# Kernel tuning notes

Measured on AMD Instinct MI355X. Metric: run time of the kernel, lower is better.

## Reference

```python
import jax, jax.numpy as jnp
import numpy as np

EPS = 1e-6
R_DEPTH = 12   # CONFIG['max_recursion_depth']
STACK = 48     # CONFIG['stack_size']
GB, CG, CC = 0.8, 2.0, 0.25  # graph_bias_scale, context_gate_strength, commitment_cost


def _g(k, shape, s=0.05):
    return (jax.random.normal(k, shape) * s).astype(jnp.float32)


def setup_inputs():
    D, V, B, S = 128, 16384, 32, 128
    NS, NM = 64, 128
    ks = iter(jax.random.split(jax.random.key(0), 40))
    return {
        "input_ids": jax.random.randint(next(ks), (B, S), 0, V),
        "prev_syn_idx": jax.random.randint(next(ks), (B,), 0, NS),
        "prev_sem_idx": jax.random.randint(next(ks), (B,), 0, NM),
        "emb_mag": _g(next(ks), (V, D), 1.0),
        "emb_phase": _g(next(ks), (V, D), 1.0),
        "cell_Wr": _g(next(ks), (D, D)), "cell_Wi": _g(next(ks), (D, D)),
        "norm_scale": jnp.ones((D,), jnp.float32),
        "norm_shift": jnp.zeros((D,), jnp.float32),
        "modrelu_b": jnp.zeros((D,), jnp.float32),
        "qWr": _g(next(ks), (D, D)), "qWi": _g(next(ks), (D, D)),
        "kWr": _g(next(ks), (D, D)), "kWi": _g(next(ks), (D, D)),
        "vWr": _g(next(ks), (D, D)), "vWi": _g(next(ks), (D, D)),
        "oWr": _g(next(ks), (D, D)), "oWi": _g(next(ks), (D, D)),
        "halt_W": _g(next(ks), (2 * D, 1)),
        "halt_b": jnp.full((1,), -2.0, jnp.float32),  # nn.init.constant_(halt_linear.bias, -2.0)
        "stk_W": _g(next(ks), (2 * D, 3)), "stk_b": jnp.zeros((3,), jnp.float32),
        "cb_syn": _g(next(ks), (64, 2 * D), 1.0),
        "cb_sem": _g(next(ks), (128, 2 * D), 1.0),
        "ctxsyn_W": _g(next(ks), (2 * D, NS)), "ctxsyn_b": jnp.zeros((NS,), jnp.float32),
        "ctxsem_W": _g(next(ks), (2 * D, NM)), "ctxsem_b": jnp.zeros((NM,), jnp.float32),
        "adj_syn": _g(next(ks), (NS, NS), 1.0),
        "adj_sem": _g(next(ks), (NM, NM), 1.0),
        "gate_W": _g(next(ks), (4 * D, D)), "gate_b": jnp.zeros((D,), jnp.float32),
        "dec_W": _g(next(ks), (2 * D, V)), "dec_b": jnp.zeros((V,), jnp.float32),
    }


def _forward(fl, input_ids, prev_syn_idx, prev_sem_idx):
    (emb_mag, emb_phase, cell_Wr, cell_Wi, norm_scale, norm_shift, modrelu_b,
     qWr, qWi, kWr, kWi, vWr, vWi, oWr, oWi, halt_W, halt_b, stk_W, stk_b,
     cb_syn, cb_sem, ctxsyn_W, ctxsyn_b, ctxsem_W, ctxsem_b, adj_syn, adj_sem,
     gate_W, gate_b, dec_W, dec_b) = fl
    B = input_ids.shape[0]
    D = emb_mag.shape[1]
    sg = jax.lax.stop_gradient

    def clin(r, i, Wr, Wi):  # ComplexLinear (no bias)
        return r @ Wr - i @ Wi, i @ Wr + r @ Wi

    def cell(zr, zi):  # AdaptiveRecursiveCell
        r, i = clin(zr, zi, cell_Wr, cell_Wi)
        # ComplexLayerNorm (torch.var is unbiased -> ddof=1)
        mag = jnp.sqrt(r * r + i * i) + EPS
        mean = mag.mean(-1, keepdims=True)
        var = jnp.var(mag, axis=-1, ddof=1, keepdims=True)
        nm = (mag - mean) / jnp.sqrt(var + EPS) * norm_scale + norm_shift
        r, i = nm * r / mag, nm * i / mag  # cos/sin of original phase
        # ModReLU
        n = jnp.sqrt(r * r + i * i) + EPS
        s = jax.nn.relu(n + modrelu_b) / n
        r, i = r * s, i * s
        # MultiHeadComplexAttention: source computes Q,K but out = V -> o_proj(v_proj(z))
        vr, vi = clin(r, i, vWr, vWi)
        r, i = clin(vr, vi, oWr, oWi)
        zf = jnp.concatenate([r, i], -1)
        halt = jax.nn.sigmoid(zf @ halt_W + halt_b)          # [B,1]
        ctrl = jax.nn.softmax(zf @ stk_W + stk_b, axis=-1)   # [B,3]
        return r, i, halt, ctrl

    def stack_step(zr, zi, mem, ptr, ctrl):  # DifferentiableStack
        push, pop, noop = ctrl[:, 0:1], ctrl[:, 1:2], ctrl[:, 2:3]
        pu, pd = jnp.roll(ptr, 1, axis=1), jnp.roll(ptr, -1, axis=1)
        nptr = push * pu + pop * pd + noop * ptr
        nptr = nptr / (nptr.sum(1, keepdims=True) + EPS)
        zf = jnp.concatenate([zr, zi], -1)
        wm = (push * pu)[:, :, None]                          # write mask [B,STACK,1]
        mem = wm * zf[:, None, :] + mem * (1.0 - wm)
        read = (mem * nptr[:, :, None]).sum(1)                # [B,2D]
        return read[:, :D], read[:, D:], mem, nptr

    def gres(zr, zi, sr, si):  # GatedResidual, g_c = g + i*g
        g = jax.nn.sigmoid(jnp.concatenate([zr, zi, sr, si], -1) @ gate_W + gate_b)
        return ((1.0 - g) * zr + g * zi + g * (sr - si),
                (1.0 - g) * zi - g * zr + g * (si + sr))

    def vq(zr, zi, cb, adj, cW, cbias, pidx):  # ContextAwareDualVQ.vq_step (eval mode)
        zf = jnp.concatenate([zr, zi], -1)                    # [B,2D]
        d = (zf * zf).sum(1, keepdims=True) + (cb * cb).sum(1) - 2.0 * zf @ cb.T
        d = d - GB * jax.nn.sigmoid(adj[pidx]) - CG * jax.nn.softmax(zf @ cW + cbias, -1)
        idx = jnp.argmin(d, axis=1)
        zq = cb[idx]
        loss = jnp.mean((sg(zq) - zf) ** 2) + CC * jnp.mean((zq - sg(zf)) ** 2)
        return zf + sg(zq - zf), loss, idx                    # STE

    def step(carry, ids_t):
        mem, ptr, psyn, psem, lacc = carry
        r, th = emb_mag[ids_t], emb_phase[ids_t]              # embed
        zr, zi = r * jnp.cos(th), r * jnp.sin(th)
        rem = jnp.ones((B, 1), zr.dtype)
        accr = jnp.zeros_like(zr); acci = jnp.zeros_like(zi)
        slr = jnp.zeros_like(zr); sli = jnp.zeros_like(zi)
        for n in range(R_DEPTH):  # ACT recursion, halting-weighted accumulation
            pr, pi, halt, ctrl = cell(zr, zi)
            rr, ri, mem, ptr = stack_step(pr, pi, mem, ptr, ctrl)
            zr, zi = gres(pr, pi, rr, ri)
            w = rem if n == R_DEPTH - 1 else rem * halt
            accr, acci = accr + w * zr, acci + w * zi
            rem = rem * (1.0 - halt)
            slr, sli = slr + zr / R_DEPTH, sli + zi / R_DEPTH
        zqs, ls, isyn = vq(accr, acci, cb_syn, adj_syn, ctxsyn_W, ctxsyn_b, psyn)
        zqm, lm, isem = vq(slr, sli, cb_sem, adj_sem, ctxsem_W, ctxsem_b, psem)
        logits = 0.5 * (zqs + zqm) @ dec_W + dec_b            # decoder: Linear(2D, V)
        return (mem, ptr, isyn, isem, lacc + ls + lm), logits

    mem0 = jnp.zeros((B, STACK, 2 * D), jnp.float32)
    ptr0 = jnp.zeros((B, STACK), jnp.float32).at[:, 0].set(1.0)
    carry0 = (mem0, ptr0, prev_syn_idx, prev_sem_idx, jnp.zeros((), jnp.float32))
    (_, _, _, _, vq_loss), logits = jax.lax.scan(step, carry0, input_ids.T)
    return jnp.transpose(logits, (1, 0, 2)), vq_loss          # [B,S,V], scalar


def reference(input_ids, prev_syn_idx, prev_sem_idx, emb_mag, emb_phase, cell_Wr, cell_Wi, norm_scale, norm_shift, modrelu_b, qWr, qWi, kWr, kWi, vWr, vWi, oWr, oWi, halt_W, halt_b, stk_W, stk_b, cb_syn, cb_sem, ctxsyn_W, ctxsyn_b, ctxsem_W, ctxsem_b, adj_syn, adj_sem, gate_W, gate_b, dec_W, dec_b):
    fl = (emb_mag, emb_phase, cell_Wr, cell_Wi, norm_scale, norm_shift, modrelu_b,
          qWr, qWi, kWr, kWi, vWr, vWi, oWr, oWi, halt_W, halt_b, stk_W, stk_b,
          cb_syn, cb_sem, ctxsyn_W, ctxsyn_b, ctxsem_W, ctxsem_b, adj_syn, adj_sem,
          gate_W, gate_b, dec_W, dec_b)
    return _forward(fl, input_ids, prev_syn_idx, prev_sem_idx)
```

## Files before the change

### kernel.cpp

```cpp
#include <hip/hip_runtime.h>
#include <hip/hip_fp16.h>
#include <math.h>

#define D 128
#define D2 256
#define STK 48
#define SEQ 128
#define BATCH 32
#define RDPT 12
#define NSYN 64
#define NSEM 128
#define VOC 16384
#define EPSF 1e-6f
#define GB_C 0.8f
#define CG_C 2.0f

struct RParams {
  const int* input_ids;
  const int* prev_syn;
  const int* prev_sem;
  const float* emb_mag;
  const float* emb_phase;
  const float* cell_Wr;
  const float* cell_Wi;
  const float* norm_scale;
  const float* norm_shift;
  const float* modrelu_b;
  const float* VOr;
  const float* VOi;
  const float* halt_W;
  const float* halt_b;
  const float* stk_W;
  const float* stk_b;
  const float* cb_syn;
  const float* cb_sem;
  const float* ctxsyn_W;
  const float* ctxsyn_b;
  const float* ctxsem_W;
  const float* ctxsem_b;
  const float* gate_b;
  const uint4* gatePk;
  const float* cbT_syn;
  const float* cbT_sem;
  const float* cnrm_syn;
  const float* cnrm_sem;
  const float* gbsig_syn;
  const float* gbsig_sem;
  float* X;
  float* lossp;
};

__device__ __forceinline__ float waveAllSum(float v) {
  #pragma unroll
  for (int m = 32; m; m >>= 1) v += __shfl_xor(v, m);
  return v;
}

__global__ __launch_bounds__(512, 2) void recur_kernel(RParams p) {
  __shared__ uint4 gateLds[64 * D];
  __shared__ float partr[512], parti[512];
  __shared__ alignas(16) float xr_[D], xi_[D], cr_[D], ci_[D];
  __shared__ float rAiA[D2], marr[D];
  __shared__ alignas(16) float zfc[D2], rd_[D2];
  __shared__ alignas(16) float acc2[D2], sl2[D2];
  __shared__ float zqs[D2];
  __shared__ float sptr[STK];
  __shared__ alignas(16) float nptrs[STK], wms[STK];
  __shared__ float hW_s[D2];
  __shared__ float stW_s[D2 * 3];
  __shared__ float scal[16];
  __shared__ int icb[2];
  __shared__ int ids[SEQ];

  const int tid = threadIdx.x;
  const int b = blockIdx.x;
  const int wv = tid >> 6;
  const int l = tid & 63;
  const int j = tid & 127;
  const int kq = tid >> 7;
  const int k0 = kq * 32;

  float cwr[32], cwi[32], owr[32], owi[32];
  #pragma unroll
  for (int kk = 0; kk < 32; ++kk) {
    cwr[kk] = p.cell_Wr[(size_t)(k0 + kk) * D + j];
    cwi[kk] = p.cell_Wi[(size_t)(k0 + kk) * D + j];
    owr[kk] = p.VOr[(size_t)(k0 + kk) * D + j];
    owi[kk] = p.VOi[(size_t)(k0 + kk) * D + j];
  }
  for (int e = tid; e < 64 * D; e += 512) gateLds[e] = p.gatePk[e];
  float snsR = 0.f, nshR = 0.f, smbR = 0.f, sgbR = 0.f;
  if (tid < D) {
    snsR = p.norm_scale[tid];
    nshR = p.norm_shift[tid];
    smbR = p.modrelu_b[tid];
    sgbR = p.gate_b[tid];
  }
  if (tid < D2) hW_s[tid] = p.halt_W[tid];
  for (int e = tid; e < D2 * 3; e += 512) stW_s[e] = p.stk_W[e];
  if (tid < SEQ) ids[tid] = p.input_ids[(size_t)b * SEQ + tid];
  if (tid < STK) sptr[tid] = (tid == 0) ? 1.f : 0.f;
  if (tid == 0) { icb[0] = p.prev_syn[b]; icb[1] = p.prev_sem[b]; }
  const float hb = p.halt_b[0];
  const float sb0 = p.stk_b[0], sb1 = p.stk_b[1], sb2 = p.stk_b[2];

  float memv[24];
  #pragma unroll
  for (int q = 0; q < 24; ++q) memv[q] = 0.f;
  const int mdl = tid & 255, mjh = tid >> 8;
  float lossAcc = 0.f;
  float remv = 1.f;
  float mNxt = 0.f, pNxt = 0.f;
  __syncthreads();

  if (tid < D) {
    const int id0 = ids[0];
    mNxt = p.emb_mag[(size_t)id0 * D + tid];
    pNxt = p.emb_phase[(size_t)id0 * D + tid];
  }

  for (int t = 0; t < SEQ; ++t) {
    if (tid < D) {
      float sv, cv;
      sincosf(pNxt, &sv, &cv);
      xr_[tid] = mNxt * cv;
      xi_[tid] = mNxt * sv;
    }
    float accR = 0.f, accI = 0.f, slR = 0.f, slI = 0.f;
    if (tid < 64) remv = 1.f;
    __syncthreads();

    for (int n = 0; n < RDPT; ++n) {
      {
        const float4* x4r = (const float4*)(&xr_[k0]);
        const float4* x4i = (const float4*)(&xi_[k0]);
        float a0 = 0.f, a1 = 0.f, a2 = 0.f, a3 = 0.f;
        #pragma unroll
        for (int q = 0; q < 8; ++q) {
          float4 xa = x4r[q];
          float4 xb = x4i[q];
          a0 = fmaf(xa.x, cwr[q*4+0], a0); a0 = fmaf(-xb.x, cwi[q*4+0], a0);
          a1 = fmaf(xb.x, cwr[q*4+0], a1); a1 = fmaf(xa.x, cwi[q*4+0], a1);
          a2 = fmaf(xa.y, cwr[q*4+1], a2); a2 = fmaf(-xb.y, cwi[q*4+1], a2);
          a3 = fmaf(xb.y, cwr[q*4+1], a3); a3 = fmaf(xa.y, cwi[q*4+1], a3);
          a0 = fmaf(xa.z, cwr[q*4+2], a0); a0 = fmaf(-xb.z, cwi[q*4+2], a0);
          a1 = fmaf(xb.z, cwr[q*4+2], a1); a1 = fmaf(xa.z, cwi[q*4+2], a1);
          a2 = fmaf(xa.w, cwr[q*4+3], a2); a2 = fmaf(-xb.w, cwi[q*4+3], a2);
          a3 = fmaf(xb.w, cwr[q*4+3], a3); a3 = fmaf(xa.w, cwi[q*4+3], a3);
        }
        partr[tid] = a0 + a2;
        parti[tid] = a1 + a3;
      }
      __syncthreads();
      if (tid < D) {
        float rr = partr[tid] + partr[tid + 128] + partr[tid + 256] + partr[tid + 384];
        float ii = parti[tid] + parti[tid + 128] + parti[tid + 256] + parti[tid + 384];
        rAiA[tid] = rr;
        rAiA[tid + 128] = ii;
        marr[tid] = sqrtf(rr * rr + ii * ii) + EPSF;
      }
      __syncthreads();
      if (tid < 64) {
        float m0 = marr[l], m1 = marr[l + 64];
        float mean = waveAllSum(m0 + m1) * (1.f / D);
        float d0 = m0 - mean, d1 = m1 - mean;
        float v = waveAllSum(d0 * d0 + d1 * d1);
        if (l == 0) {
          scal[1] = mean;
          scal[2] = rsqrtf(v * (1.f / (D - 1)) + EPSF);
        }
      }
      __syncthreads();
      if (tid < D) {
        float m = marr[tid];
        float nm = (m - scal[1]) * scal[2] * snsR + nshR;
        float r_ = nm * rAiA[tid] / m;
        float i_ = nm * rAiA[tid + 128] / m;
        float nn = sqrtf(r_ * r_ + i_ * i_) + EPSF;
        float sc = fmaxf(nn + smbR, 0.f) / nn;
        cr_[tid] = r_ * sc;
        ci_[tid] = i_ * sc;
      }
      __syncthreads();
      {
        const float4* c4r = (const float4*)(&cr_[k0]);
        const float4* c4i = (const float4*)(&ci_[k0]);
        float a0 = 0.f, a1 = 0.f, a2 = 0.f, a3 = 0.f;
        #pragma unroll
        for (int q = 0; q < 8; ++q) {
          float4 xa = c4r[q];
          float4 xb = c4i[q];
          a0 = fmaf(xa.x, owr[q*4+0], a0); a0 = fmaf(-xb.x, owi[q*4+0], a0);
          a1 = fmaf(xb.x, owr[q*4+0], a1); a1 = fmaf(xa.x, owi[q*4+0], a1);
          a2 = fmaf(xa.y, owr[q*4+1], a2); a2 = fmaf(-xb.y, owi[q*4+1], a2);
          a3 = fmaf(xb.y, owr[q*4+1], a3); a3 = fmaf(xa.y, owi[q*4+1], a3);
          a0 = fmaf(xa.z, owr[q*4+2], a0); a0 = fmaf(-xb.z, owi[q*4+2], a0);
          a1 = fmaf(xb.z, owr[q*4+2], a1); a1 = fmaf(xa.z, owi[q*4+2], a1);
          a2 = fmaf(xa.w, owr[q*4+3], a2); a2 = fmaf(-xb.w, owi[q*4+3], a2);
          a3 = fmaf(xb.w, owr[q*4+3], a3); a3 = fmaf(xa.w, owi[q*4+3], a3);
        }
        partr[tid] = a0 + a2;
        parti[tid] = a1 + a3;
      }
      __syncthreads();
      if (tid < 256) {
        if (tid < 128) {
          zfc[tid] = partr[tid] + partr[tid + 128] + partr[tid + 256] + partr[tid + 384];
        } else {
          const int d = tid - 128;
          zfc[tid] = parti[d] + parti[d + 128] + parti[d + 256] + parti[d + 384];
        }
      }
      __syncthreads();
      if (tid < 256) {
        float z0 = zfc[l], z1 = zfc[l + 64], z2 = zfc[l + 128], z3 = zfc[l + 192];
        float s;
        if (wv == 0) {
          s = z0 * hW_s[l] + z1 * hW_s[l + 64] + z2 * hW_s[l + 128] + z3 * hW_s[l + 192];
        } else {
          const int c = wv - 1;
          s = z0 * stW_s[l * 3 + c] + z1 * stW_s[(l + 64) * 3 + c] +
              z2 * stW_s[(l + 128) * 3 + c] + z3 * stW_s[(l + 192) * 3 + c];
        }
        s = waveAllSum(s);
        if (l == 0) scal[4 + wv] = s;
      }
      __syncthreads();
      if (tid < 64) {
        float halt = 1.f / (1.f + expf(-(scal[4] + hb)));
        float e0 = scal[5] + sb0, e1 = scal[6] + sb1, e2 = scal[7] + sb2;
        float mx = fmaxf(e0, fmaxf(e1, e2));
        float x0 = expf(e0 - mx), x1 = expf(e1 - mx), x2 = expf(e2 - mx);
        float sm = x0 + x1 + x2;
        float push = x0 / sm, pop = x1 / sm, noop = x2 / sm;
        float wgt = (n == RDPT - 1) ? remv : remv * halt;
        if (l == 0) scal[3] = wgt;
        remv = remv * (1.f - halt);
        float pj = 0.f, pu = 0.f, pd = 0.f;
        if (l < STK) {
          pj = sptr[l];
          pu = sptr[(l + STK - 1) % STK];
          pd = sptr[(l + 1) % STK];
        }
        float np_ = push * pu + pop * pd + noop * pj;
        float wm_ = push * pu;
        float ssum = waveAllSum((l < STK) ? np_ : 0.f);
        float inv = 1.f / (ssum + EPSF);
        if (l < STK) {
          np_ *= inv;
          nptrs[l] = np_;
          sptr[l] = np_;
          wms[l] = wm_;
        }
      }
      __syncthreads();
      {
        const float4* wm4 = (const float4*)wms;
        const float4* np4 = (const float4*)nptrs;
        float zfd = zfc[mdl];
        float accA = 0.f, accB = 0.f;
        #pragma unroll
        for (int m4 = 0; m4 < 6; ++m4) {
          float4 wmv = wm4[mjh * 6 + m4];
          float4 npv = np4[mjh * 6 + m4];
          const int base = m4 * 4;
          memv[base + 0] = wmv.x * zfd + memv[base + 0] * (1.f - wmv.x);
          accA = fmaf(memv[base + 0], npv.x, accA);
          memv[base + 1] = wmv.y * zfd + memv[base + 1] * (1.f - wmv.y);
          accB = fmaf(memv[base + 1], npv.y, accB);
          memv[base + 2] = wmv.z * zfd + memv[base + 2] * (1.f - wmv.z);
          accA = fmaf(memv[base + 2], npv.z, accA);
          memv[base + 3] = wmv.w * zfd + memv[base + 3] * (1.f - wmv.w);
          accB = fmaf(memv[base + 3], npv.w, accB);
        }
        partr[tid] = accA + accB;
      }
      __syncthreads();
      if (tid < D2) rd_[tid] = partr[tid] + partr[tid + 256];
      __syncthreads();
      {
        const float4* s4 = (kq < 2) ? (const float4*)(&zfc[kq * 128])
                                    : (const float4*)(&rd_[(kq - 2) * 128]);
        const uint4* g16 = &gateLds[(kq * 16) * D + j];
        float g0 = 0.f, g1 = 0.f, g2 = 0.f, g3 = 0.f;
        #pragma unroll
        for (int o = 0; o < 16; ++o) {
          float4 xa = s4[2 * o];
          float4 xb = s4[2 * o + 1];
          uint4 w = g16[(size_t)o * D];
          union { unsigned u; __half2 h; } c0, c1, c2, c3;
          c0.u = w.x; c1.u = w.y; c2.u = w.z; c3.u = w.w;
          float2 f0 = __half22float2(c0.h);
          float2 f1 = __half22float2(c1.h);
          float2 f2 = __half22float2(c2.h);
          float2 f3 = __half22float2(c3.h);
          g0 = fmaf(xa.x, f0.x, g0); g1 = fmaf(xa.y, f0.y, g1);
          g2 = fmaf(xa.z, f1.x, g2); g3 = fmaf(xa.w, f1.y, g3);
          g0 = fmaf(xb.x, f2.x, g0); g1 = fmaf(xb.y, f2.y, g1);
          g2 = fmaf(xb.z, f3.x, g2); g3 = fmaf(xb.w, f3.y, g3);
        }
        partr[tid] = (g0 + g1) + (g2 + g3);
      }
      __syncthreads();
      if (tid < D) {
        float g = partr[tid] + partr[tid + 128] + partr[tid + 256] +
                  partr[tid + 384] + sgbR;
        g = 1.f / (1.f + expf(-g));
        float pr_ = zfc[tid], pi_ = zfc[tid + 128];
        float rr_ = rd_[tid], ri_ = rd_[tid + 128];
        float nzr = (1.f - g) * pr_ + g * pi_ + g * (rr_ - ri_);
        float nzi = (1.f - g) * pi_ - g * pr_ + g * (ri_ + rr_);
        xr_[tid] = nzr;
        xi_[tid] = nzi;
        float wgt = scal[3];
        accR += wgt * nzr;
        accI += wgt * nzi;
        slR += nzr * (1.f / RDPT);
        slI += nzi * (1.f / RDPT);
      }
      __syncthreads();
    }

    if (tid < D) {
      const int idn = ids[(t + 1 < SEQ) ? t + 1 : t];
      mNxt = p.emb_mag[(size_t)idn * D + tid];
      pNxt = p.emb_phase[(size_t)idn * D + tid];
    }
    if (tid < D) {
      acc2[tid] = accR; acc2[tid + 128] = accI;
      sl2[tid] = slR;  sl2[tid + 128] = slI;
    }
    __syncthreads();

    {
      const int c = tid & 63, ch = tid >> 6;
      const int kb = ch * 32;
      const float* cb = p.cbT_syn + (size_t)kb * 64 + c;
      const float* cw = p.ctxsyn_W + (size_t)kb * 64 + c;
      const float4* a4 = (const float4*)(&acc2[kb]);
      float d0 = 0.f, d1 = 0.f, e0 = 0.f, e1 = 0.f;
      #pragma unroll
      for (int q = 0; q < 8; ++q) {
        float4 zv = a4[q];
        d0 = fmaf(cb[(size_t)(q * 4 + 0) * 64], zv.x, d0);
        e0 = fmaf(cw[(size_t)(q * 4 + 0) * 64], zv.x, e0);
        d1 = fmaf(cb[(size_t)(q * 4 + 1) * 64], zv.y, d1);
        e1 = fmaf(cw[(size_t)(q * 4 + 1) * 64], zv.y, e1);
        d0 = fmaf(cb[(size_t)(q * 4 + 2) * 64], zv.z, d0);
        e0 = fmaf(cw[(size_t)(q * 4 + 2) * 64], zv.z, e0);
        d1 = fmaf(cb[(size_t)(q * 4 + 3) * 64], zv.w, d1);
        e1 = fmaf(cw[(size_t)(q * 4 + 3) * 64], zv.w, e1);
      }
      partr[ch * 64 + c] = d0 + d1;
      parti[ch * 64 + c] = e0 + e1;
    }
    __syncthreads();
    if (tid < 64) {
      float dot = 0.f, e = p.ctxsyn_b[l];
      #pragma unroll
      for (int ch = 0; ch < 8; ++ch) {
        dot += partr[ch * 64 + l];
        e += parti[ch * 64 + l];
      }
      float d = p.cnrm_syn[l] - 2.f * dot;
      float m = e;
      #pragma unroll
      for (int mm = 32; mm; mm >>= 1) m = fmaxf(m, __shfl_xor(m, mm));
      float ex = expf(e - m);
      float s = waveAllSum(ex);
      const int pidx = icb[0];
      float score = d - p.gbsig_syn[(size_t)pidx * 64 + l] - CG_C * (ex / s);
      float bv = score; int bi = l;
      #pragma unroll
      for (int mm = 32; mm; mm >>= 1) {
        float ov = __shfl_xor(bv, mm); int oi = __shfl_xor(bi, mm);
        if (ov < bv || (ov == bv && oi < bi)) { bv = ov; bi = oi; }
      }
      if (l == 0) icb[0] = bi;
    }
    __syncthreads();
    if (tid < D2) {
      const int idx = icb[0];
      float zqv = p.cb_syn[(size_t)idx * D2 + tid];
      float df = zqv - acc2[tid];
      lossAcc += df * df;
      zqs[tid] = zqv;
    }
    {
      const int c = tid & 127, ch = tid >> 7;
      const int kb = ch * 64;
      const float* cb = p.cbT_sem + (size_t)kb * 128 + c;
      const float* cw = p.ctxsem_W + (size_t)kb * 128 + c;
      const float4* a4 = (const float4*)(&sl2[kb]);
      float d0 = 0.f, d1 = 0.f, e0 = 0.f, e1 = 0.f;
      #pragma unroll
      for (int q = 0; q < 16; ++q) {
        float4 zv = a4[q];
        d0 = fmaf(cb[(size_t)(q * 4 + 0) * 128], zv.x, d0);
        e0 = fmaf(cw[(size_t)(q * 4 + 0) * 128], zv.x, e0);
        d1 = fmaf(cb[(size_t)(q * 4 + 1) * 128], zv.y, d1);
        e1 = fmaf(cw[(size_t)(q * 4 + 1) * 128], zv.y, e1);
        d0 = fmaf(cb[(size_t)(q * 4 + 2) * 128], zv.z, d0);
        e0 = fmaf(cw[(size_t)(q * 4 + 2) * 128], zv.z, e0);
        d1 = fmaf(cb[(size_t)(q * 4 + 3) * 128], zv.w, d1);
        e1 = fmaf(cw[(size_t)(q * 4 + 3) * 128], zv.w, e1);
      }
      partr[ch * 128 + c] = d0 + d1;
      parti[ch * 128 + c] = e0 + e1;
    }
    __syncthreads();
    if (tid < 64) {
      float dot0 = 0.f, e0 = p.ctxsem_b[l];
      float dot1 = 0.f, e1 = p.ctxsem_b[l + 64];
      #pragma unroll
      for (int ch = 0; ch < 4; ++ch) {
        dot0 += partr[ch * 128 + l];       e0 += parti[ch * 128 + l];
        dot1 += partr[ch * 128 + l + 64];  e1 += parti[ch * 128 + l + 64];
      }
      float d0 = p.cnrm_sem[l] - 2.f * dot0;
      float d1 = p.cnrm_sem[l + 64] - 2.f * dot1;
      float m = fmaxf(e0, e1);
      #pragma unroll
      for (int mm = 32; mm; mm >>= 1) m = fmaxf(m, __shfl_xor(m, mm));
      float x0 = expf(e0 - m), x1 = expf(e1 - m);
      float s = waveAllSum(x0 + x1);
      const int pidx = icb[1];
      float s0 = d0 - p.gbsig_sem[(size_t)pidx * 128 + l] - CG_C * (x0 / s);
      float s1 = d1 - p.gbsig_sem[(size_t)pidx * 128 + l + 64] - CG_C * (x1 / s);
      float bv = s0; int bi = l;
      if (s1 < bv) { bv = s1; bi = l + 64; }
      #pragma unroll
      for (int mm = 32; mm; mm >>= 1) {
        float ov = __shfl_xor(bv, mm); int oi = __shfl_xor(bi, mm);
        if (ov < bv || (ov == bv && oi < bi)) { bv = ov; bi = oi; }
      }
      if (l == 0) icb[1] = bi;
    }
    __syncthreads();
    if (tid < D2) {
      const int idx = icb[1];
      float zqv = p.cb_sem[(size_t)idx * D2 + tid];
      float df = zqv - sl2[tid];
      lossAcc += df * df;
      p.X[(size_t)(b * SEQ + t) * D2 + tid] = 0.5f * (zqs[tid] + zqv);
    }
    __syncthreads();
  }

  partr[tid] = lossAcc;
  __syncthreads();
  if (tid < 256) partr[tid] += partr[tid + 256];
  __syncthreads();
  if (tid < 128) partr[tid] += partr[tid + 128];
  __syncthreads();
  if (tid < 64) {
    float v = partr[tid] + partr[tid + 64];
    v = waveAllSum(v);
    if (tid == 0) p.lossp[b] = v;
  }
}

__global__ __launch_bounds__(256) void voprod_kernel(const float* __restrict__ vr,
                                                     const float* __restrict__ vi,
                                                     const float* __restrict__ orr,
                                                     const float* __restrict__ oii,
                                                     float* __restrict__ VOr,
                                                     float* __restrict__ VOi) {
  __shared__ float a_r[D], a_i[D];
  const int k = blockIdx.x;
  const int tid = threadIdx.x;
  if (tid < D) { a_r[tid] = vr[k * D + tid]; a_i[tid] = vi[k * D + tid]; }
  __syncthreads();
  const int m = tid & 127;
  const int half = tid >> 7;
  float acc = 0.f;
  if (half == 0) {
    #pragma unroll 8
    for (int jj = 0; jj < D; ++jj)
      acc += a_r[jj] * orr[jj * D + m] - a_i[jj] * oii[jj * D + m];
    VOr[k * D + m] = acc;
  } else {
    #pragma unroll 8
    for (int jj = 0; jj < D; ++jj)
      acc += a_r[jj] * oii[jj * D + m] + a_i[jj] * orr[jj * D + m];
    VOi[k * D + m] = acc;
  }
}

__global__ void vqprep_kernel(const float* __restrict__ cb_syn,
                              const float* __restrict__ cb_sem,
                              const float* __restrict__ adj_syn,
                              const float* __restrict__ adj_sem,
                              const float* __restrict__ gate_W,
                              float* __restrict__ cbT_syn,
                              float* __restrict__ cbT_sem,
                              float* __restrict__ cnrm_syn,
                              float* __restrict__ cnrm_sem,
                              float* __restrict__ gbsig_syn,
                              float* __restrict__ gbsig_sem,
                              uint4* __restrict__ gatePk) {
  const int tid = blockIdx.x * 256 + threadIdx.x;
  const int nt = gridDim.x * 256;
  for (int e = tid; e < NSYN * D2; e += nt) {
    int c = e / D2, k = e % D2;
    cbT_syn[k * NSYN + c] = cb_syn[e];
  }
  for (int e = tid; e < NSEM * D2; e += nt) {
    int c = e / D2, k = e % D2;
    cbT_sem[k * NSEM + c] = cb_sem[e];
  }
  for (int c = tid; c < NSYN; c += nt) {
    float s = 0.f;
    for (int k = 0; k < D2; ++k) { float v = cb_syn[c * D2 + k]; s += v * v; }
    cnrm_syn[c] = s;
  }
  for (int c = tid; c < NSEM; c += nt) {
    float s = 0.f;
    for (int k = 0; k < D2; ++k) { float v = cb_sem[c * D2 + k]; s += v * v; }
    cnrm_sem[c] = s;
  }
  for (int e = tid; e < NSYN * NSYN; e += nt)
    gbsig_syn[e] = GB_C / (1.f + expf(-adj_syn[e]));
  for (int e = tid; e < NSEM * NSEM; e += nt)
    gbsig_sem[e] = GB_C / (1.f + expf(-adj_sem[e]));
  for (int e = tid; e < 64 * D; e += nt) {
    int o = e / D, jj = e % D;
    union { unsigned u; __half2 h; } w0, w1, w2, w3;
    w0.h = __halves2half2(__float2half(gate_W[(size_t)(8 * o + 0) * D + jj]),
                          __float2half(gate_W[(size_t)(8 * o + 1) * D + jj]));
    w1.h = __halves2half2(__float2half(gate_W[(size_t)(8 * o + 2) * D + jj]),
                          __float2half(gate_W[(size_t)(8 * o + 3) * D + jj]));
    w2.h = __halves2half2(__float2half(gate_W[(size_t)(8 * o + 4) * D + jj]),
                          __float2half(gate_W[(size_t)(8 * o + 5) * D + jj]));
    w3.h = __halves2half2(__float2half(gate_W[(size_t)(8 * o + 6) * D + jj]),
                          __float2half(gate_W[(size_t)(8 * o + 7) * D + jj]));
    uint4 pk;
    pk.x = w0.u; pk.y = w1.u; pk.z = w2.u; pk.w = w3.u;
    gatePk[e] = pk;
  }
}

__global__ __launch_bounds__(256) void dec_kernel(const float* __restrict__ X,
                                                  const float* __restrict__ W,
                                                  const float* __restrict__ bias,
                                                  float* __restrict__ out) {
  __shared__ float A[32][D2];
  const int tid = threadIdx.x;
  const int bx = blockIdx.x;
  const int by = blockIdx.y;
  const float* xr = X + (size_t)by * 32 * D2;
  #pragma unroll
  for (int s = 0; s < 32; ++s) A[s][tid] = xr[s * D2 + tid];
  __syncthreads();
  const int ty = tid >> 5, tx = tid & 31;
  const int col0 = bx * 128 + tx * 4;
  const int r0 = ty * 4;
  float acc[4][4];
  #pragma unroll
  for (int r = 0; r < 4; ++r) {
    acc[r][0] = 0.f; acc[r][1] = 0.f; acc[r][2] = 0.f; acc[r][3] = 0.f;
  }
  const float* wp = W + col0;
  for (int k = 0; k < D2; k += 4) {
    float4 w0 = *(const float4*)(wp + (size_t)(k + 0) * VOC);
    float4 w1 = *(const float4*)(wp + (size_t)(k + 1) * VOC);
    float4 w2 = *(const float4*)(wp + (size_t)(k + 2) * VOC);
    float4 w3 = *(const float4*)(wp + (size_t)(k + 3) * VOC);
    #pragma unroll
    for (int r = 0; r < 4; ++r) {
      float4 a = *(const float4*)&A[r0 + r][k];
      acc[r][0] += a.x * w0.x + a.y * w1.x + a.z * w2.x + a.w * w3.x;
      acc[r][1] += a.x * w0.y + a.y * w1.y + a.z * w2.y + a.w * w3.y;
      acc[r][2] += a.x * w0.z + a.y * w1.z + a.z * w2.z + a.w * w3.z;
      acc[r][3] += a.x * w0.w + a.y * w1.w + a.z * w2.w + a.w * w3.w;
    }
  }
  float4 bv = *(const float4*)(bias + col0);
  #pragma unroll
  for (int r = 0; r < 4; ++r) {
    float4 o;
    o.x = acc[r][0] + bv.x; o.y = acc[r][1] + bv.y;
    o.z = acc[r][2] + bv.z; o.w = acc[r][3] + bv.w;
    *(float4*)(out + (size_t)(by * 32 + r0 + r) * VOC + col0) = o;
  }
}

__global__ void loss_kernel(const float* __restrict__ lp, float* __restrict__ out) {
  int l = threadIdx.x;
  float v = (l < BATCH) ? lp[l] : 0.f;
  #pragma unroll
  for (int off = 32; off; off >>= 1) v += __shfl_down(v, off);
  if (l == 0) out[0] = v * (1.25f / 8192.f);
}

extern "C" void kernel_launch(void* const* d_in, const int* in_sizes, int n_in,
                              void* d_out, int out_size, void* d_ws,
                              size_t ws_size, hipStream_t stream) {
  float* ws = (float*)d_ws;
  float* X = ws;
  float* lossp = X + 1048576;
  float* VOr = lossp + 64;
  float* VOi = VOr + 16384;
  float* cbT_syn = VOi + 16384;
  float* cbT_sem = cbT_syn + 16384;
  float* cnrm_syn = cbT_sem + 32768;
  float* cnrm_sem = cnrm_syn + 64;
  float* gbsig_syn = cnrm_sem + 128;
  float* gbsig_sem = gbsig_syn + 4096;
  uint4* gatePk = (uint4*)(gbsig_sem + 16384);

  RParams p;
  p.input_ids  = (const int*)d_in[0];
  p.prev_syn   = (const int*)d_in[1];
  p.prev_sem   = (const int*)d_in[2];
  p.emb_mag    = (const float*)d_in[3];
  p.emb_phase  = (const float*)d_in[4];
  p.cell_Wr    = (const float*)d_in[5];
  p.cell_Wi    = (const float*)d_in[6];
  p.norm_scale = (const float*)d_in[7];
  p.norm_shift = (const float*)d_in[8];
  p.modrelu_b  = (const float*)d_in[9];
  p.VOr        = VOr;
  p.VOi        = VOi;
  p.halt_W     = (const float*)d_in[18];
  p.halt_b     = (const float*)d_in[19];
  p.stk_W      = (const float*)d_in[20];
  p.stk_b      = (const float*)d_in[21];
  p.cb_syn     = (const float*)d_in[22];
  p.cb_sem     = (const float*)d_in[23];
  p.ctxsyn_W   = (const float*)d_in[24];
  p.ctxsyn_b   = (const float*)d_in[25];
  p.ctxsem_W   = (const float*)d_in[26];
  p.ctxsem_b   = (const float*)d_in[27];
  p.gate_b     = (const float*)d_in[31];
  p.gatePk     = gatePk;
  const float* gate_W = (const float*)d_in[30];
  const float* dec_W = (const float*)d_in[32];
  const float* dec_b = (const float*)d_in[33];
  p.cbT_syn = cbT_syn;
  p.cbT_sem = cbT_sem;
  p.cnrm_syn = cnrm_syn;
  p.cnrm_sem = cnrm_sem;
  p.gbsig_syn = gbsig_syn;
  p.gbsig_sem = gbsig_sem;
  p.X = X;
  p.lossp = lossp;

  float* out = (float*)d_out;

  voprod_kernel<<<D, 256, 0, stream>>>((const float*)d_in[14], (const float*)d_in[15],
                                       (const float*)d_in[16], (const float*)d_in[17],
                                       VOr, VOi);
  vqprep_kernel<<<64, 256, 0, stream>>>((const float*)d_in[22], (const float*)d_in[23],
                                        (const float*)d_in[28], (const float*)d_in[29],
                                        gate_W, cbT_syn, cbT_sem, cnrm_syn,
                                        cnrm_sem, gbsig_syn, gbsig_sem, gatePk);
  recur_kernel<<<BATCH, 512, 0, stream>>>(p);
  dec_kernel<<<dim3(VOC / 128, BATCH * SEQ / 32), 256, 0, stream>>>(X, dec_W,
                                                                    dec_b, out);
  loss_kernel<<<1, 64, 0, stream>>>(lossp, out + (size_t)BATCH * SEQ * VOC);
}
```

Baseline: 15.46 ms.

## Merge recurrent-step stages to remove block barriers in recur_kernel

Collapses the magnitude, layer-norm and modReLU stages into a single wavefront that reduces the partial sums directly. Wave 4 computes the halt and stack logits from the raw partials while other waves build zfc, so that stage no longer waits on an extra barrier. The per-token syntactic and semantic codebook stages are interleaved using a second partial buffer, and the next token's embedding is computed at the end of the step instead of at the start. The aim is fewer __syncthreads in this latency-bound serial loop. In exchange it uses more shared memory, loads the same LDS data redundantly, and swaps sincosf for the lower-precision __sincosf.

```diff
diff --git a/kernel.cpp b/kernel.cpp
--- a/kernel.cpp
+++ b/kernel.cpp
@@ -59,8 +59,8 @@
 __global__ __launch_bounds__(512, 2) void recur_kernel(RParams p) {
   __shared__ uint4 gateLds[64 * D];
   __shared__ float partr[512], parti[512];
+  __shared__ float part2r[512], part2i[512];
   __shared__ alignas(16) float xr_[D], xi_[D], cr_[D], ci_[D];
-  __shared__ float rAiA[D2], marr[D];
   __shared__ alignas(16) float zfc[D2], rd_[D2];
   __shared__ alignas(16) float acc2[D2], sl2[D2];
   __shared__ float zqs[D2];
@@ -68,7 +68,8 @@
   __shared__ alignas(16) float nptrs[STK], wms[STK];
   __shared__ float hW_s[D2];
   __shared__ float stW_s[D2 * 3];
-  __shared__ float scal[16];
+  __shared__ float sns_s[D], nsh_s[D], smb_s[D];
+  __shared__ float scal[8];
   __shared__ int icb[2];
   __shared__ int ids[SEQ];
 
@@ -89,12 +90,11 @@
     owi[kk] = p.VOi[(size_t)(k0 + kk) * D + j];
   }
   for (int e = tid; e < 64 * D; e += 512) gateLds[e] = p.gatePk[e];
-  float snsR = 0.f, nshR = 0.f, smbR = 0.f, sgbR = 0.f;
+  const float sgbR = (tid < D) ? p.gate_b[tid] : 0.f;
   if (tid < D) {
-    snsR = p.norm_scale[tid];
-    nshR = p.norm_shift[tid];
-    smbR = p.modrelu_b[tid];
-    sgbR = p.gate_b[tid];
+    sns_s[tid] = p.norm_scale[tid];
+    nsh_s[tid] = p.norm_shift[tid];
+    smb_s[tid] = p.modrelu_b[tid];
   }
   if (tid < D2) hW_s[tid] = p.halt_W[tid];
   for (int e = tid; e < D2 * 3; e += 512) stW_s[e] = p.stk_W[e];
@@ -117,18 +117,16 @@
     const int id0 = ids[0];
     mNxt = p.emb_mag[(size_t)id0 * D + tid];
     pNxt = p.emb_phase[(size_t)id0 * D + tid];
-  }
+    float sv, cv;
+    __sincosf(pNxt, &sv, &cv);
+    xr_[tid] = mNxt * cv;
+    xi_[tid] = mNxt * sv;
+  }
+  __syncthreads();
 
   for (int t = 0; t < SEQ; ++t) {
-    if (tid < D) {
-      float sv, cv;
-      sincosf(pNxt, &sv, &cv);
-      xr_[tid] = mNxt * cv;
-      xi_[tid] = mNxt * sv;
-    }
     float accR = 0.f, accI = 0.f, slR = 0.f, slI = 0.f;
-    if (tid < 64) remv = 1.f;
-    __syncthreads();
+    if (wv == 4) remv = 1.f;
 
     for (int n = 0; n < RDPT; ++n) {
       {
@@ -152,34 +150,30 @@
         parti[tid] = a1 + a3;
       }
       __syncthreads();
-      if (tid < D) {
-        float rr = partr[tid] + partr[tid + 128] + partr[tid + 256] + partr[tid + 384];
-        float ii = parti[tid] + parti[tid + 128] + parti[tid + 256] + parti[tid + 384];
-        rAiA[tid] = rr;
-        rAiA[tid + 128] = ii;
-        marr[tid] = sqrtf(rr * rr + ii * ii) + EPSF;
-      }
-      __syncthreads();
       if (tid < 64) {
-        float m0 = marr[l], m1 = marr[l + 64];
+        float rr0 = 0.f, ii0 = 0.f, rr1 = 0.f, ii1 = 0.f;
+        #pragma unroll
+        for (int q = 0; q < 4; ++q) {
+          rr0 += partr[l + q * 128];       ii0 += parti[l + q * 128];
+          rr1 += partr[l + 64 + q * 128];  ii1 += parti[l + 64 + q * 128];
+        }
+        float m0 = sqrtf(rr0 * rr0 + ii0 * ii0) + EPSF;
+        float m1 = sqrtf(rr1 * rr1 + ii1 * ii1) + EPSF;
         float mean = waveAllSum(m0 + m1) * (1.f / D);
-        float d0 = m0 - mean, d1 = m1 - mean;
-        float v = waveAllSum(d0 * d0 + d1 * d1);
-        if (l == 0) {
-          scal[1] = mean;
-          scal[2] = rsqrtf(v * (1.f / (D - 1)) + EPSF);
-        }
-      }
-      __syncthreads();
-      if (tid < D) {
-        float m = marr[tid];
-        float nm = (m - scal[1]) * scal[2] * snsR + nshR;
-        float r_ = nm * rAiA[tid] / m;
-        float i_ = nm * rAiA[tid + 128] / m;
-        float nn = sqrtf(r_ * r_ + i_ * i_) + EPSF;
-        float sc = fmaxf(nn + smbR, 0.f) / nn;
-        cr_[tid] = r_ * sc;
-        ci_[tid] = i_ * sc;
+        float dd0 = m0 - mean, dd1 = m1 - mean;
+        float istd = rsqrtf(waveAllSum(dd0 * dd0 + dd1 * dd1) * (1.f / (D - 1)) + EPSF);
+        float nm0 = (m0 - mean) * istd * sns_s[l] + nsh_s[l];
+        float r0_ = nm0 * rr0 / m0, i0_ = nm0 * ii0 / m0;
+        float nn0 = sqrtf(r0_ * r0_ + i0_ * i0_) + EPSF;
+        float sc0 = fmaxf(nn0 + smb_s[l], 0.f) / nn0;
+        cr_[l] = r0_ * sc0;
+        ci_[l] = i0_ * sc0;
+        float nm1 = (m1 - mean) * istd * sns_s[l + 64] + nsh_s[l + 64];
+        float r1_ = nm1 * rr1 / m1, i1_ = nm1 * ii1 / m1;
+        float nn1 = sqrtf(r1_ * r1_ + i1_ * i1_) + EPSF;
+        float sc1 = fmaxf(nn1 + smb_s[l + 64], 0.f) / nn1;
+        cr_[l + 64] = r1_ * sc1;
+        ci_[l + 64] = i1_ * sc1;
       }
       __syncthreads();
       {
@@ -210,25 +204,24 @@
           const int d = tid - 128;
           zfc[tid] = parti[d] + parti[d + 128] + parti[d + 256] + parti[d + 384];
         }
-      }
-      __syncthreads();
-      if (tid < 256) {
-        float z0 = zfc[l], z1 = zfc[l + 64], z2 = zfc[l + 128], z3 = zfc[l + 192];
-        float s;
-        if (wv == 0) {
-          s = z0 * hW_s[l] + z1 * hW_s[l + 64] + z2 * hW_s[l + 128] + z3 * hW_s[l + 192];
-        } else {
-          const int c = wv - 1;
-          s = z0 * stW_s[l * 3 + c] + z1 * stW_s[(l + 64) * 3 + c] +
-              z2 * stW_s[(l + 128) * 3 + c] + z3 * stW_s[(l + 192) * 3 + c];
-        }
-        s = waveAllSum(s);
-        if (l == 0) scal[4 + wv] = s;
-      }
-      __syncthreads();
-      if (tid < 64) {
-        float halt = 1.f / (1.f + expf(-(scal[4] + hb)));
-        float e0 = scal[5] + sb0, e1 = scal[6] + sb1, e2 = scal[7] + sb2;
+      } else if (wv == 4) {
+        float sh = 0.f, s0 = 0.f, s1 = 0.f, s2 = 0.f;
+        #pragma unroll
+        for (int q = 0; q < 8; ++q) {
+          const int e = l + 64 * q;
+          const int d = e & 127;
+          float pr = partr[e], pi = parti[e];
+          sh = fmaf(pr, hW_s[d], sh);          sh = fmaf(pi, hW_s[d + 128], sh);
+          s0 = fmaf(pr, stW_s[d * 3 + 0], s0); s0 = fmaf(pi, stW_s[(d + 128) * 3 + 0], s0);
+          s1 = fmaf(pr, stW_s[d * 3 + 1], s1); s1 = fmaf(pi, stW_s[(d + 128) * 3 + 1], s1);
+          s2 = fmaf(pr, stW_s[d * 3 + 2], s2); s2 = fmaf(pi, stW_s[(d + 128) * 3 + 2], s2);
+        }
+        sh = waveAllSum(sh);
+        s0 = waveAllSum(s0);
+        s1 = waveAllSum(s1);
+        s2 = waveAllSum(s2);
+        float halt = 1.f / (1.f + expf(-(sh + hb)));
+        float e0 = s0 + sb0, e1 = s1 + sb1, e2 = s2 + sb2;
         float mx = fmaxf(e0, fmaxf(e1, e2));
         float x0 = expf(e0 - mx), x1 = expf(e1 - mx), x2 = expf(e2 - mx);
         float sm = x0 + x1 + x2;
@@ -317,6 +310,10 @@
         accI += wgt * nzi;
         slR += nzr * (1.f / RDPT);
         slI += nzi * (1.f / RDPT);
+        if (n == RDPT - 1) {
+          acc2[tid] = accR; acc2[tid + 128] = accI;
+          sl2[tid] = slR;  sl2[tid + 128] = slI;
+        }
       }
       __syncthreads();
     }
@@ -326,12 +323,6 @@
       mNxt = p.emb_mag[(size_t)idn * D + tid];
       pNxt = p.emb_phase[(size_t)idn * D + tid];
     }
-    if (tid < D) {
-      acc2[tid] = accR; acc2[tid + 128] = accI;
-      sl2[tid] = slR;  sl2[tid + 128] = slI;
-    }
-    __syncthreads();
-
     {
       const int c = tid & 63, ch = tid >> 6;
       const int kb = ch * 32;
@@ -354,38 +345,6 @@
       partr[ch * 64 + c] = d0 + d1;
       parti[ch * 64 + c] = e0 + e1;
     }
-    __syncthreads();
-    if (tid < 64) {
-      float dot = 0.f, e = p.ctxsyn_b[l];
-      #pragma unroll
-      for (int ch = 0; ch < 8; ++ch) {
-        dot += partr[ch * 64 + l];
-        e += parti[ch * 64 + l];
-      }
-      float d = p.cnrm_syn[l] - 2.f * dot;
-      float m = e;
-      #pragma unroll
-      for (int mm = 32; mm; mm >>= 1) m = fmaxf(m, __shfl_xor(m, mm));
-      float ex = expf(e - m);
-      float s = waveAllSum(ex);
-      const int pidx = icb[0];
-      float score = d - p.gbsig_syn[(size_t)pidx * 64 + l] - CG_C * (ex / s);
-      float bv = score; int bi = l;
-      #pragma unroll
-      for (int mm = 32; mm; mm >>= 1) {
-        float ov = __shfl_xor(bv, mm); int oi = __shfl_xor(bi, mm);
-        if (ov < bv || (ov == bv && oi < bi)) { bv = ov; bi = oi; }
-      }
-      if (l == 0) icb[0] = bi;
-    }
-    __syncthreads();
-    if (tid < D2) {
-      const int idx = icb[0];
-      float zqv = p.cb_syn[(size_t)idx * D2 + tid];
-      float df = zqv - acc2[tid];
-      lossAcc += df * df;
-      zqs[tid] = zqv;
-    }
     {
       const int c = tid & 127, ch = tid >> 7;
       const int kb = ch * 64;
@@ -405,8 +364,32 @@
         d1 = fmaf(cb[(size_t)(q * 4 + 3) * 128], zv.w, d1);
         e1 = fmaf(cw[(size_t)(q * 4 + 3) * 128], zv.w, e1);
       }
-      partr[ch * 128 + c] = d0 + d1;
-      parti[ch * 128 + c] = e0 + e1;
+      part2r[ch * 128 + c] = d0 + d1;
+      part2i[ch * 128 + c] = e0 + e1;
+    }
+    __syncthreads();
+    if (tid < 64) {
+      float dot = 0.f, e = p.ctxsyn_b[l];
+      #pragma unroll
+      for (int ch = 0; ch < 8; ++ch) {
+        dot += partr[ch * 64 + l];
+        e += parti[ch * 64 + l];
+      }
+      float d = p.cnrm_syn[l] - 2.f * dot;
+      float m = e;
+      #pragma unroll
+      for (int mm = 32; mm; mm >>= 1) m = fmaxf(m, __shfl_xor(m, mm));
+      float ex = expf(e - m);
+      float s = waveAllSum(ex);
+      const int pidx = icb[0];
+      float score = d - p.gbsig_syn[(size_t)pidx * 64 + l] - CG_C * (ex / s);
+      float bv = score; int bi = l;
+      #pragma unroll
+      for (int mm = 32; mm; mm >>= 1) {
+        float ov = __shfl_xor(bv, mm); int oi = __shfl_xor(bi, mm);
+        if (ov < bv || (ov == bv && oi < bi)) { bv = ov; bi = oi; }
+      }
+      if (l == 0) icb[0] = bi;
     }
     __syncthreads();
     if (tid < 64) {
@@ -414,8 +397,8 @@
       float dot1 = 0.f, e1 = p.ctxsem_b[l + 64];
       #pragma unroll
       for (int ch = 0; ch < 4; ++ch) {
-        dot0 += partr[ch * 128 + l];       e0 += parti[ch * 128 + l];
-        dot1 += partr[ch * 128 + l + 64];  e1 += parti[ch * 128 + l + 64];
+        dot0 += part2r[ch * 128 + l];       e0 += part2i[ch * 128 + l];
+        dot1 += part2r[ch * 128 + l + 64];  e1 += part2i[ch * 128 + l + 64];
       }
       float d0 = p.cnrm_sem[l] - 2.f * dot0;
       float d1 = p.cnrm_sem[l + 64] - 2.f * dot1;
@@ -435,6 +418,13 @@
         if (ov < bv || (ov == bv && oi < bi)) { bv = ov; bi = oi; }
       }
       if (l == 0) icb[1] = bi;
+    } else if (tid >= 256) {
+      const int d = tid - 256;
+      const int idx = icb[0];
+      float zqv = p.cb_syn[(size_t)idx * D2 + d];
+      float df = zqv - acc2[d];
+      lossAcc += df * df;
+      zqs[d] = zqv;
     }
     __syncthreads();
     if (tid < D2) {
@@ -443,6 +433,12 @@
       float df = zqv - sl2[tid];
       lossAcc += df * df;
       p.X[(size_t)(b * SEQ + t) * D2 + tid] = 0.5f * (zqs[tid] + zqv);
+    }
+    if (tid < D) {
+      float sv, cv;
+      __sincosf(pNxt, &sv, &cv);
+      xr_[tid] = mNxt * cv;
+      xi_[tid] = mNxt * sv;
     }
     __syncthreads();
   }
```

Result: slower. 16.97 ms (+9.8%).
